# Optimization experiments

Measured on AMD Instinct MI355X. Metric: run time of the kernel, lower is better.

## Reference

```python
import jax, jax.numpy as jnp
import numpy as np

H = 16      # n_heads
D = 1024    # d_model
DK = D // H # head dim


def setup_inputs() -> dict:
    key = jax.random.key(0)
    ks = jax.random.split(key, 11)
    B, S = 4, 2048
    std = 1.0 / np.sqrt(D)
    inp = {
        "query": jax.random.normal(ks[0], (B, S, D), jnp.float32),
        "key": jax.random.normal(ks[1], (B, S, D), jnp.float32),
        "value": jax.random.normal(ks[2], (B, S, D), jnp.float32),
        "Wq": jax.random.normal(ks[3], (D, D), jnp.float32) * std,
        "bq": jnp.zeros((D,), jnp.float32),
        "Wk": jax.random.normal(ks[4], (D, D), jnp.float32) * std,
        "bk": jnp.zeros((D,), jnp.float32),
        "Wv": jax.random.normal(ks[5], (D, D), jnp.float32) * std,
        "bv": jnp.zeros((D,), jnp.float32),
        "Wo": jax.random.normal(ks[6], (D, D), jnp.float32) * std,
        "bo": jnp.zeros((D,), jnp.float32),
    }
    return inp


def reference(query, key, value, Wq, bq, Wk, bk, Wv, bv, Wo, bo):
    B, S, _ = query.shape
    # QKV projections (nn.Linear), then split heads: [B, S, H, DK]
    q = (query @ Wq + bq).reshape(B, S, H, DK)
    k = (key @ Wk + bk).reshape(B, S, H, DK)
    v = (value @ Wv + bv).reshape(B, S, H, DK)
    # Memory-efficient attention computes exactly softmax(QK^T/sqrt(dk))V
    scale = 1.0 / np.sqrt(DK).astype(np.float32)
    scores = jnp.einsum("bqhd,bkhd->bhqk", q, k) * scale  # [B, H, S, S]
    attn = jax.nn.softmax(scores, axis=-1)
    x = jnp.einsum("bhqk,bkhd->bqhd", attn, v)            # [B, S, H, DK]
    x = x.reshape(B, S, H * DK)
    return x @ Wo + bo
```

## Files before the change

kernel.cpp:

```cpp
#include <hip/hip_runtime.h>
#include <hip/hip_bf16.h>

typedef short short8 __attribute__((ext_vector_type(8)));
typedef float f32x4 __attribute__((ext_vector_type(4)));
typedef float f32x16 __attribute__((ext_vector_type(16)));
typedef unsigned short u16;
typedef unsigned int u32;

#define HD 16
#define DMODEL 1024
#define DKH 64
#define SEQ 2048
#define QSCALE 0.18033688f

typedef const __attribute__((address_space(1))) void gvoid;
typedef __attribute__((address_space(3))) void lvoid;

__device__ inline u16 f2bf(float f) {
  unsigned int x = __builtin_bit_cast(unsigned int, f);
  unsigned int r = (x + 0x7fffu + ((x >> 16) & 1u)) >> 16;
  return (u16)r;
}

__device__ inline float fexp2(float x) {
#if __has_builtin(__builtin_amdgcn_exp2f)
  return __builtin_amdgcn_exp2f(x);
#else
  return __expf(x * 0.69314718f);
#endif
}

__device__ inline u32 cvtpk(float lo, float hi_) {
  u32 r;
  asm("v_cvt_pk_bf16_f32 %0, %1, %2" : "=v"(r) : "v"(lo), "v"(hi_));
  return r;
}

__device__ inline f32x4 mfma16(short8 a, short8 b, f32x4 c) {
  return __builtin_amdgcn_mfma_f32_16x16x32_bf16(a, b, c, 0, 0, 0);
}
__device__ inline f32x16 mfma32(short8 a, short8 b, f32x16 c) {
  return __builtin_amdgcn_mfma_f32_32x32x16_bf16(a, b, c, 0, 0, 0);
}

__global__ __launch_bounds__(256) void wt_kernel(const float* __restrict__ W0,
                                                 const float* __restrict__ W1,
                                                 const float* __restrict__ W2,
                                                 const float* __restrict__ W3,
                                                 u16* __restrict__ T) {
  __shared__ float tile[64][65];
  const float* W = blockIdx.z == 0 ? W0 : blockIdx.z == 1 ? W1 : blockIdx.z == 2 ? W2 : W3;
  u16* out = T + (size_t)blockIdx.z * DMODEL * DMODEL;
  int n0 = blockIdx.x * 64, k0 = blockIdx.y * 64;
  int tx = threadIdx.x & 63, ty = threadIdx.x >> 6;
  for (int i = 0; i < 16; i++) {
    int r = ty + i * 4;
    tile[r][tx] = W[(size_t)(k0 + r) * DMODEL + n0 + tx];
  }
  __syncthreads();
  for (int i = 0; i < 16; i++) {
    int r = ty + i * 4;
    out[(size_t)(n0 + r) * DMODEL + k0 + tx] = f2bf(tile[tx][r]);
  }
}

__global__ __launch_bounds__(256, 3) void gemm_qkv(const float* __restrict__ q,
                                                   const float* __restrict__ k,
                                                   const float* __restrict__ v,
                                                   const u16* __restrict__ WT,
                                                   const float* __restrict__ bq,
                                                   const float* __restrict__ bk,
                                                   const float* __restrict__ bv,
                                                   u16* __restrict__ Qb,
                                                   u16* __restrict__ Kb,
                                                   u16* __restrict__ Vtb) {
  __shared__ u16 As[128 * 64];
  __shared__ u16 Bs[128 * 64];
  const int b = blockIdx.x;
  const int xcd = b & 7, slot = b >> 3;
  const int nidx = slot & 7, pl = slot >> 3;
  const int pg = xcd * 24 + pl;
  const int z = pg >> 6, by = pg & 63;

  const float* A = z == 0 ? q : z == 1 ? k : v;
  const u16* Bt = WT + (size_t)z * DMODEL * DMODEL;
  const float* bias = z == 0 ? bq : z == 1 ? bk : bv;
  u16* Cv = z == 0 ? Qb : z == 1 ? Kb : Vtb;
  const float scale = z == 0 ? QSCALE : 1.0f;
  const bool vtrans = (z == 2);

  const int m0 = by * 128, n0 = nidx * 128;
  const int tid = threadIdx.x;
  const int lane = tid & 63, wid = tid >> 6;
  const int g = lane >> 4, c = lane & 15;
  const int wr = (wid >> 1) * 64, wc = (wid & 1) * 64;

  const int trow = tid >> 3;
  const int tcolb = (tid & 7) << 4;
  const int swr = (c & 7) << 4;
  f32x4 acc[4][4] = {};

  for (int kt = 0; kt < 16; ++kt) {
    const int k0 = kt * 64;
#pragma unroll
    for (int p = 0; p < 4; ++p) {
      const int row = p * 32 + trow;
      const int scol = tcolb ^ ((row & 7) << 4);
      __builtin_amdgcn_global_load_lds(
          (gvoid*)((const char*)Bt + ((size_t)(n0 + row) * DMODEL + k0) * 2 + scol),
          (lvoid*)((char*)Bs + row * 128 + tcolb), 16, 0, 0);
    }
#pragma unroll
    for (int p = 0; p < 4; ++p) {
      const int row = p * 32 + trow;
      const float* src = A + (size_t)(m0 + row) * DMODEL + k0 + (tid & 7) * 8;
      const float4 a0 = *(const float4*)src;
      const float4 a1 = *(const float4*)(src + 4);
      u32 tmp[4] = {cvtpk(a0.x, a0.y), cvtpk(a0.z, a0.w),
                    cvtpk(a1.x, a1.y), cvtpk(a1.z, a1.w)};
      *(uint4*)((char*)As + row * 128 + (tcolb ^ ((row & 7) << 4))) = *(uint4*)tmp;
    }
    __syncthreads();
#pragma unroll
    for (int kk = 0; kk < 2; ++kk) {
      short8 af[4], bfr[4];
#pragma unroll
      for (int mi = 0; mi < 4; ++mi)
        af[mi] = *(const short8*)((const char*)As + (wr + mi * 16 + c) * 128 + ((kk * 64 + g * 16) ^ swr));
#pragma unroll
      for (int ni = 0; ni < 4; ++ni)
        bfr[ni] = *(const short8*)((const char*)Bs + (wc + ni * 16 + c) * 128 + ((kk * 64 + g * 16) ^ swr));
#pragma unroll
      for (int mi = 0; mi < 4; ++mi)
#pragma unroll
        for (int ni = 0; ni < 4; ++ni)
          acc[mi][ni] = mfma16(af[mi], bfr[ni], acc[mi][ni]);
    }
    __syncthreads();
  }

  for (int ni = 0; ni < 4; ++ni) {
    const int colg = n0 + wc + ni * 16 + c;
    const float bv_ = bias[colg];
    for (int mi = 0; mi < 4; ++mi) {
      const int rowb = m0 + wr + mi * 16 + g * 4;
      const int bb = rowb >> 11, s = rowb & 2047;
      const int h = colg >> 6, dk = colg & 63;
      if (!vtrans) {
        const size_t base = ((size_t)(bb * HD + h)) * SEQ;
        for (int j = 0; j < 4; ++j)
          Cv[(base + s + j) * DKH + dk] = f2bf((acc[mi][ni][j] + bv_) * scale);
      } else {
        const size_t base = ((size_t)(bb * HD + h) * DKH + dk) * SEQ + s;
        ushort4 u;
        u.x = f2bf(acc[mi][ni][0] + bv_);
        u.y = f2bf(acc[mi][ni][1] + bv_);
        u.z = f2bf(acc[mi][ni][2] + bv_);
        u.w = f2bf(acc[mi][ni][3] + bv_);
        *(ushort4*)(&Cv[base]) = u;
      }
    }
  }
}

__global__ __launch_bounds__(256, 3) void gemm_out(const u16* __restrict__ A,
                                                   const u16* __restrict__ Bt,
                                                   const float* __restrict__ bias,
                                                   float* __restrict__ C) {
  __shared__ u16 As[128 * 64];
  __shared__ u16 Bs[128 * 64];
  const int b = blockIdx.x;
  const int xcd = b & 7, slot = b >> 3;
  const int nidx = slot & 7, pl = slot >> 3;
  const int by = xcd * 8 + pl;

  const int m0 = by * 128, n0 = nidx * 128;
  const int tid = threadIdx.x;
  const int lane = tid & 63, wid = tid >> 6;
  const int g = lane >> 4, c = lane & 15;
  const int wr = (wid >> 1) * 64, wc = (wid & 1) * 64;

  const int trow = tid >> 3;
  const int tcolb = (tid & 7) << 4;
  const int swr = (c & 7) << 4;
  f32x4 acc[4][4] = {};

  for (int kt = 0; kt < 16; ++kt) {
    const int k0 = kt * 64;
#pragma unroll
    for (int p = 0; p < 4; ++p) {
      const int row = p * 32 + trow;
      const int scol = tcolb ^ ((row & 7) << 4);
      __builtin_amdgcn_global_load_lds(
          (gvoid*)((const char*)A + ((size_t)(m0 + row) * DMODEL + k0) * 2 + scol),
          (lvoid*)((char*)As + row * 128 + tcolb), 16, 0, 0);
      __builtin_amdgcn_global_load_lds(
          (gvoid*)((const char*)Bt + ((size_t)(n0 + row) * DMODEL + k0) * 2 + scol),
          (lvoid*)((char*)Bs + row * 128 + tcolb), 16, 0, 0);
    }
    __syncthreads();
#pragma unroll
    for (int kk = 0; kk < 2; ++kk) {
      short8 af[4], bfr[4];
#pragma unroll
      for (int mi = 0; mi < 4; ++mi)
        af[mi] = *(const short8*)((const char*)As + (wr + mi * 16 + c) * 128 + ((kk * 64 + g * 16) ^ swr));
#pragma unroll
      for (int ni = 0; ni < 4; ++ni)
        bfr[ni] = *(const short8*)((const char*)Bs + (wc + ni * 16 + c) * 128 + ((kk * 64 + g * 16) ^ swr));
#pragma unroll
      for (int mi = 0; mi < 4; ++mi)
#pragma unroll
        for (int ni = 0; ni < 4; ++ni)
          acc[mi][ni] = mfma16(af[mi], bfr[ni], acc[mi][ni]);
    }
    __syncthreads();
  }

  for (int ni = 0; ni < 4; ++ni) {
    const int colg = n0 + wc + ni * 16 + c;
    const float bv = bias[colg];
    for (int mi = 0; mi < 4; ++mi) {
      const int rowb = m0 + wr + mi * 16 + g * 4;
      for (int j = 0; j < 4; ++j)
        C[(size_t)(rowb + j) * DMODEL + colg] = acc[mi][ni][j] + bv;
    }
  }
}

__global__ __launch_bounds__(256, 4) void attn_kernel(const u16* __restrict__ Q,
                                                      const u16* __restrict__ K,
                                                      const u16* __restrict__ Vt,
                                                      u16* __restrict__ X) {
  __shared__ char ldsmem[2][2][8192];
  const int tid = threadIdx.x;
  const int lane = tid & 63, wid = tid >> 6;
  const int c5 = lane & 31, hi = lane >> 5;

  const int blk = blockIdx.x;
  const int work = (blk & 7) * 128 + (blk >> 3);
  const int qt = work & 15, bh = work >> 4;

  const int q0 = qt * 128 + wid * 32;
  const u16* qb = Q + (size_t)bh * SEQ * DKH;
  const char* kbB = (const char*)(K + (size_t)bh * SEQ * DKH);
  const char* vbB = (const char*)(Vt + (size_t)bh * DKH * SEQ);

  short8 qf[4];
#pragma unroll
  for (int ks = 0; ks < 4; ++ks)
    qf[ks] = *(const short8*)(qb + (size_t)(q0 + c5) * DKH + ks * 16 + hi * 8);

  const int srow = tid >> 3;
  const int scolb = (tid & 7) << 4;
  const int scol = scolb ^ ((srow & 7) << 4);

  const int fswz = (c5 & 7) << 4;
  int cofs[4];
#pragma unroll
  for (int ks = 0; ks < 4; ++ks) cofs[ks] = ((ks * 32 + hi * 16) ^ fswz);

  f32x16 oacc[2] = {};
  float mrun = -1e30f, lrun = 0.f;

#pragma unroll
  for (int r32 = 0; r32 < 64; r32 += 32) {
    __builtin_amdgcn_global_load_lds(
        (gvoid*)(kbB + (size_t)(r32 + srow) * 128 + scol),
        (lvoid*)(&ldsmem[0][0][(r32 + srow) * 128 + scolb]), 16, 0, 0);
    __builtin_amdgcn_global_load_lds(
        (gvoid*)(vbB + (size_t)(r32 + srow) * (SEQ * 2) + scol),
        (lvoid*)(&ldsmem[0][1][(r32 + srow) * 128 + scolb]), 16, 0, 0);
  }
  __syncthreads();

#pragma unroll 2
  for (int t = 0; t < 32; ++t) {
    const int buf = t & 1;
    if (t < 31) {
      const size_t kv1 = (size_t)(t + 1) * 64;
#pragma unroll
      for (int r32 = 0; r32 < 64; r32 += 32) {
        __builtin_amdgcn_global_load_lds(
            (gvoid*)(kbB + (kv1 + r32 + srow) * 128 + scol),
            (lvoid*)(&ldsmem[buf ^ 1][0][(r32 + srow) * 128 + scolb]), 16, 0, 0);
        __builtin_amdgcn_global_load_lds(
            (gvoid*)(vbB + (size_t)(r32 + srow) * (SEQ * 2) + kv1 * 2 + scol),
            (lvoid*)(&ldsmem[buf ^ 1][1][(r32 + srow) * 128 + scolb]), 16, 0, 0);
      }
    }

    const char* bK = &ldsmem[buf][0][0];
    const char* bV = &ldsmem[buf][1][0];

    f32x16 sacc[2] = {};
#pragma unroll
    for (int kt = 0; kt < 2; ++kt) {
      short8 kf[4];
#pragma unroll
      for (int ks = 0; ks < 4; ++ks)
        kf[ks] = *(const short8*)(bK + (kt * 32 + c5) * 128 + cofs[ks]);
#pragma unroll
      for (int ks = 0; ks < 4; ++ks)
        sacc[kt] = mfma32(kf[ks], qf[ks], sacc[kt]);
    }

    float pm = sacc[0][0];
#pragma unroll
    for (int kt = 0; kt < 2; ++kt)
#pragma unroll
      for (int r = 0; r < 16; ++r) pm = fmaxf(pm, sacc[kt][r]);
    pm = fmaxf(pm, __shfl_xor(pm, 32, 64));

    if (!__all(pm <= mrun + 11.5f)) {
      float mnew = fmaxf(mrun, pm);
      float a = fexp2(mrun - mnew);
      mrun = mnew;
      lrun *= a;
#pragma unroll
      for (int r = 0; r < 16; ++r) {
        float ar = __shfl(a, (r & 3) + 8 * (r >> 2) + 4 * hi, 64);
        oacc[0][r] *= ar;
        oacc[1][r] *= ar;
      }
    }
    float rs = 0.f;
#pragma unroll
    for (int kt = 0; kt < 2; ++kt)
#pragma unroll
      for (int r = 0; r < 16; ++r) {
        float p = fexp2(sacc[kt][r] - mrun);
        sacc[kt][r] = p;
        rs += p;
      }
    rs += __shfl_xor(rs, 32, 64);
    lrun += rs;

    u32 W[2][8], Xw[2][8];
#pragma unroll
    for (int kt = 0; kt < 2; ++kt)
#pragma unroll
      for (int j = 0; j < 8; ++j) {
        W[kt][j] = cvtpk(sacc[kt][2 * j], sacc[kt][2 * j + 1]);
        Xw[kt][j] = __shfl_xor(W[kt][j], 32, 64);
      }
    short8 pa[4];
#pragma unroll
    for (int ks = 0; ks < 4; ++ks) {
      const int kt = ks >> 1, l4 = (ks & 1) * 4;
      u32 m0 = hi ? Xw[kt][l4 + 2] : W[kt][l4 + 0];
      u32 m1 = hi ? Xw[kt][l4 + 3] : W[kt][l4 + 1];
      u32 m2 = hi ? W[kt][l4 + 2] : Xw[kt][l4 + 0];
      u32 m3 = hi ? W[kt][l4 + 3] : Xw[kt][l4 + 1];
      u32 tmp[4] = {m0, m1, m2, m3};
      pa[ks] = *(const short8*)tmp;
    }

    short8 vf[2][4];
#pragma unroll
    for (int dkt = 0; dkt < 2; ++dkt)
#pragma unroll
      for (int ks = 0; ks < 4; ++ks)
        vf[dkt][ks] = *(const short8*)(bV + (dkt * 32 + c5) * 128 + cofs[ks]);
#pragma unroll
    for (int ks = 0; ks < 4; ++ks)
#pragma unroll
      for (int dkt = 0; dkt < 2; ++dkt)
        oacc[dkt] = mfma32(pa[ks], vf[dkt][ks], oacc[dkt]);

    __syncthreads();
  }

  const int b = bh >> 4, h = bh & 15;
  const float inv = 1.0f / lrun;
#pragma unroll
  for (int r = 0; r < 16; ++r) {
    const int qrow = (r & 3) + 8 * (r >> 2) + 4 * hi;
    const float linv = __shfl(inv, qrow, 64);
    const size_t rowbase = ((size_t)(b * SEQ) + q0 + qrow) * DMODEL + h * DKH;
#pragma unroll
    for (int dkt = 0; dkt < 2; ++dkt)
      X[rowbase + dkt * 32 + c5] = f2bf(oacc[dkt][r] * linv);
  }
}

extern "C" void kernel_launch(void* const* d_in, const int* in_sizes, int n_in,
                              void* d_out, int out_size, void* d_ws, size_t ws_size,
                              hipStream_t stream) {
  (void)in_sizes; (void)n_in; (void)out_size; (void)ws_size;
  const float* query = (const float*)d_in[0];
  const float* key   = (const float*)d_in[1];
  const float* value = (const float*)d_in[2];
  const float* Wq = (const float*)d_in[3];
  const float* bq = (const float*)d_in[4];
  const float* Wk = (const float*)d_in[5];
  const float* bk = (const float*)d_in[6];
  const float* Wv = (const float*)d_in[7];
  const float* bv = (const float*)d_in[8];
  const float* Wo = (const float*)d_in[9];
  const float* bo = (const float*)d_in[10];
  float* out = (float*)d_out;

  char* ws = (char*)d_ws;
  const size_t MB = 1024 * 1024;
  u16* WT  = (u16*)ws;
  u16* Qb  = (u16*)(ws + 8 * MB);
  u16* Kb  = (u16*)(ws + 24 * MB);
  u16* Vtb = (u16*)(ws + 40 * MB);
  u16* Xb  = (u16*)(ws + 56 * MB);

  wt_kernel<<<dim3(16, 16, 4), 256, 0, stream>>>(Wq, Wk, Wv, Wo, WT);
  gemm_qkv<<<dim3(1536), 256, 0, stream>>>(query, key, value, WT, bq, bk, bv, Qb, Kb, Vtb);
  attn_kernel<<<dim3(1024), 256, 0, stream>>>(Qb, Kb, Vtb, Xb);
  gemm_out<<<dim3(512), 256, 0, stream>>>(Xb, WT + 3 * 1048576, bo, out);
}
```

Measured before the change: 202.3 us.

## Double-buffer LDS tiles and prefetch A in projection GEMMs

Both the QKV projection GEMM and the output GEMM now use two LDS buffers per operand. The next K-tile is staged while MFMAs run on the current one, which removes one of the two barriers per iteration. In the QKV GEMM the fp32 activations for tile t+2 are held in registers and converted to bf16 one iteration ahead, and MFMA sections are wrapped in s_setprio. The cost is double the LDS per block and higher register pressure, so occupancy hints drop from 3 to 2 blocks per CU.

```diff
diff --git a/kernel.cpp b/kernel.cpp
--- a/kernel.cpp
+++ b/kernel.cpp
@@ -64,7 +64,7 @@
   }
 }
 
-__global__ __launch_bounds__(256, 3) void gemm_qkv(const float* __restrict__ q,
+__global__ __launch_bounds__(256, 2) void gemm_qkv(const float* __restrict__ q,
                                                    const float* __restrict__ k,
                                                    const float* __restrict__ v,
                                                    const u16* __restrict__ WT,
@@ -74,8 +74,8 @@
                                                    u16* __restrict__ Qb,
                                                    u16* __restrict__ Kb,
                                                    u16* __restrict__ Vtb) {
-  __shared__ u16 As[128 * 64];
-  __shared__ u16 Bs[128 * 64];
+  __shared__ u16 As[2][128 * 64];
+  __shared__ u16 Bs[2][128 * 64];
   const int b = blockIdx.x;
   const int xcd = b & 7, slot = b >> 3;
   const int nidx = slot & 7, pl = slot >> 3;
@@ -99,45 +99,67 @@
   const int tcolb = (tid & 7) << 4;
   const int swr = (c & 7) << 4;
   f32x4 acc[4][4] = {};
-
-  for (int kt = 0; kt < 16; ++kt) {
-    const int k0 = kt * 64;
-#pragma unroll
-    for (int p = 0; p < 4; ++p) {
-      const int row = p * 32 + trow;
-      const int scol = tcolb ^ ((row & 7) << 4);
-      __builtin_amdgcn_global_load_lds(
-          (gvoid*)((const char*)Bt + ((size_t)(n0 + row) * DMODEL + k0) * 2 + scol),
-          (lvoid*)((char*)Bs + row * 128 + tcolb), 16, 0, 0);
-    }
-#pragma unroll
-    for (int p = 0; p < 4; ++p) {
-      const int row = p * 32 + trow;
-      const float* src = A + (size_t)(m0 + row) * DMODEL + k0 + (tid & 7) * 8;
-      const float4 a0 = *(const float4*)src;
-      const float4 a1 = *(const float4*)(src + 4);
-      u32 tmp[4] = {cvtpk(a0.x, a0.y), cvtpk(a0.z, a0.w),
-                    cvtpk(a1.x, a1.y), cvtpk(a1.z, a1.w)};
-      *(uint4*)((char*)As + row * 128 + (tcolb ^ ((row & 7) << 4))) = *(uint4*)tmp;
-    }
+  float4 ar[4][2];
+
+#define STAGE_B(buf, kk0)                                                          \
+  _Pragma("unroll") for (int p = 0; p < 4; ++p) {                                  \
+    const int row = p * 32 + trow;                                                 \
+    const int scol = tcolb ^ ((row & 7) << 4);                                     \
+    __builtin_amdgcn_global_load_lds(                                              \
+        (gvoid*)((const char*)Bt + ((size_t)(n0 + row) * DMODEL + (kk0)) * 2 + scol), \
+        (lvoid*)((char*)&Bs[buf][0] + row * 128 + tcolb), 16, 0, 0);               \
+  }
+#define LOAD_A(kk0)                                                                \
+  _Pragma("unroll") for (int p = 0; p < 4; ++p) {                                  \
+    const int row = p * 32 + trow;                                                 \
+    const float* src = A + (size_t)(m0 + row) * DMODEL + (kk0) + (tid & 7) * 8;    \
+    ar[p][0] = *(const float4*)src;                                                \
+    ar[p][1] = *(const float4*)(src + 4);                                          \
+  }
+#define CVT_WRITE_A(buf)                                                           \
+  _Pragma("unroll") for (int p = 0; p < 4; ++p) {                                  \
+    const int row = p * 32 + trow;                                                 \
+    u32 tmp[4] = {cvtpk(ar[p][0].x, ar[p][0].y), cvtpk(ar[p][0].z, ar[p][0].w),    \
+                  cvtpk(ar[p][1].x, ar[p][1].y), cvtpk(ar[p][1].z, ar[p][1].w)};   \
+    *(uint4*)((char*)&As[buf][0] + row * 128 + (tcolb ^ ((row & 7) << 4))) = *(uint4*)tmp; \
+  }
+
+  STAGE_B(0, 0);
+  LOAD_A(0);
+  CVT_WRITE_A(0);
+  STAGE_B(1, 64);
+  LOAD_A(64);
+  __syncthreads();
+
+  for (int t = 0; t < 16; ++t) {
+    const int cur = t & 1;
+    short8 af[4][2], bfr[4][2];
+#pragma unroll
+    for (int kk = 0; kk < 2; ++kk) {
+#pragma unroll
+      for (int mi = 0; mi < 4; ++mi)
+        af[mi][kk] = *(const short8*)((const char*)&As[cur][0] + (wr + mi * 16 + c) * 128 + ((kk * 64 + g * 16) ^ swr));
+#pragma unroll
+      for (int ni = 0; ni < 4; ++ni)
+        bfr[ni][kk] = *(const short8*)((const char*)&Bs[cur][0] + (wc + ni * 16 + c) * 128 + ((kk * 64 + g * 16) ^ swr));
+    }
+    if (t < 15) CVT_WRITE_A(cur ^ 1);
+    if (t < 14) LOAD_A((t + 2) * 64);
+    __builtin_amdgcn_s_setprio(1);
+#pragma unroll
+    for (int kk = 0; kk < 2; ++kk)
+#pragma unroll
+      for (int mi = 0; mi < 4; ++mi)
+#pragma unroll
+        for (int ni = 0; ni < 4; ++ni)
+          acc[mi][ni] = mfma16(af[mi][kk], bfr[ni][kk], acc[mi][ni]);
+    __builtin_amdgcn_s_setprio(0);
     __syncthreads();
-#pragma unroll
-    for (int kk = 0; kk < 2; ++kk) {
-      short8 af[4], bfr[4];
-#pragma unroll
-      for (int mi = 0; mi < 4; ++mi)
-        af[mi] = *(const short8*)((const char*)As + (wr + mi * 16 + c) * 128 + ((kk * 64 + g * 16) ^ swr));
-#pragma unroll
-      for (int ni = 0; ni < 4; ++ni)
-        bfr[ni] = *(const short8*)((const char*)Bs + (wc + ni * 16 + c) * 128 + ((kk * 64 + g * 16) ^ swr));
-#pragma unroll
-      for (int mi = 0; mi < 4; ++mi)
-#pragma unroll
-        for (int ni = 0; ni < 4; ++ni)
-          acc[mi][ni] = mfma16(af[mi], bfr[ni], acc[mi][ni]);
-    }
-    __syncthreads();
-  }
+    if (t < 14) STAGE_B(cur, (t + 2) * 64);
+  }
+#undef STAGE_B
+#undef LOAD_A
+#undef CVT_WRITE_A
 
   for (int ni = 0; ni < 4; ++ni) {
     const int colg = n0 + wc + ni * 16 + c;
@@ -163,12 +185,12 @@
   }
 }
 
-__global__ __launch_bounds__(256, 3) void gemm_out(const u16* __restrict__ A,
+__global__ __launch_bounds__(256, 2) void gemm_out(const u16* __restrict__ A,
                                                    const u16* __restrict__ Bt,
                                                    const float* __restrict__ bias,
                                                    float* __restrict__ C) {
-  __shared__ u16 As[128 * 64];
-  __shared__ u16 Bs[128 * 64];
+  __shared__ u16 As[2][128 * 64];
+  __shared__ u16 Bs[2][128 * 64];
   const int b = blockIdx.x;
   const int xcd = b & 7, slot = b >> 3;
   const int nidx = slot & 7, pl = slot >> 3;
@@ -185,37 +207,47 @@
   const int swr = (c & 7) << 4;
   f32x4 acc[4][4] = {};
 
-  for (int kt = 0; kt < 16; ++kt) {
-    const int k0 = kt * 64;
-#pragma unroll
-    for (int p = 0; p < 4; ++p) {
-      const int row = p * 32 + trow;
-      const int scol = tcolb ^ ((row & 7) << 4);
-      __builtin_amdgcn_global_load_lds(
-          (gvoid*)((const char*)A + ((size_t)(m0 + row) * DMODEL + k0) * 2 + scol),
-          (lvoid*)((char*)As + row * 128 + tcolb), 16, 0, 0);
-      __builtin_amdgcn_global_load_lds(
-          (gvoid*)((const char*)Bt + ((size_t)(n0 + row) * DMODEL + k0) * 2 + scol),
-          (lvoid*)((char*)Bs + row * 128 + tcolb), 16, 0, 0);
-    }
+#define STAGE_AB(buf, kk0)                                                         \
+  _Pragma("unroll") for (int p = 0; p < 4; ++p) {                                  \
+    const int row = p * 32 + trow;                                                 \
+    const int scol = tcolb ^ ((row & 7) << 4);                                     \
+    __builtin_amdgcn_global_load_lds(                                              \
+        (gvoid*)((const char*)A + ((size_t)(m0 + row) * DMODEL + (kk0)) * 2 + scol), \
+        (lvoid*)((char*)&As[buf][0] + row * 128 + tcolb), 16, 0, 0);               \
+    __builtin_amdgcn_global_load_lds(                                              \
+        (gvoid*)((const char*)Bt + ((size_t)(n0 + row) * DMODEL + (kk0)) * 2 + scol), \
+        (lvoid*)((char*)&Bs[buf][0] + row * 128 + tcolb), 16, 0, 0);               \
+  }
+
+  STAGE_AB(0, 0);
+  STAGE_AB(1, 64);
+  __syncthreads();
+
+  for (int t = 0; t < 16; ++t) {
+    const int cur = t & 1;
+    short8 af[4][2], bfr[4][2];
+#pragma unroll
+    for (int kk = 0; kk < 2; ++kk) {
+#pragma unroll
+      for (int mi = 0; mi < 4; ++mi)
+        af[mi][kk] = *(const short8*)((const char*)&As[cur][0] + (wr + mi * 16 + c) * 128 + ((kk * 64 + g * 16) ^ swr));
+#pragma unroll
+      for (int ni = 0; ni < 4; ++ni)
+        bfr[ni][kk] = *(const short8*)((const char*)&Bs[cur][0] + (wc + ni * 16 + c) * 128 + ((kk * 64 + g * 16) ^ swr));
+    }
+    __builtin_amdgcn_s_setprio(1);
+#pragma unroll
+    for (int kk = 0; kk < 2; ++kk)
+#pragma unroll
+      for (int mi = 0; mi < 4; ++mi)
+#pragma unroll
+        for (int ni = 0; ni < 4; ++ni)
+          acc[mi][ni] = mfma16(af[mi][kk], bfr[ni][kk], acc[mi][ni]);
+    __builtin_amdgcn_s_setprio(0);
     __syncthreads();
-#pragma unroll
-    for (int kk = 0; kk < 2; ++kk) {
-      short8 af[4], bfr[4];
-#pragma unroll
-      for (int mi = 0; mi < 4; ++mi)
-        af[mi] = *(const short8*)((const char*)As + (wr + mi * 16 + c) * 128 + ((kk * 64 + g * 16) ^ swr));
-#pragma unroll
-      for (int ni = 0; ni < 4; ++ni)
-        bfr[ni] = *(const short8*)((const char*)Bs + (wc + ni * 16 + c) * 128 + ((kk * 64 + g * 16) ^ swr));
-#pragma unroll
-      for (int mi = 0; mi < 4; ++mi)
-#pragma unroll
-        for (int ni = 0; ni < 4; ++ni)
-          acc[mi][ni] = mfma16(af[mi], bfr[ni], acc[mi][ni]);
-    }
-    __syncthreads();
-  }
+    if (t < 14) STAGE_AB(cur, (t + 2) * 64);
+  }
+#undef STAGE_AB
 
   for (int ni = 0; ni < 4; ++ni) {
     const int colg = n0 + wc + ni * 16 + c;
```

Measured after the change: 203.1 us. About the same (+0.4%).
